# Kernel optimization log

Hardware: AMD Instinct MI355X
Metric: run time of the kernel (lower is better)

The kernel has to match this reference:

```python
import jax, jax.numpy as jnp
import numpy as np

B, T, D, H = 8, 4096, 512, 512


def setup_inputs() -> dict:
    key = jax.random.key(0)
    k1, k2, k3, k4, k5, k6 = jax.random.split(key, 6)
    lim = 1.0 / np.sqrt(D)
    return {
        "x": jax.random.normal(k1, (B, T, D), dtype=jnp.float32),
        "h_0": jax.random.normal(k2, (B, 1, H), dtype=jnp.float32),
        "W_z": jax.random.uniform(k3, (H, D), jnp.float32, -lim, lim),
        "b_z": jax.random.uniform(k4, (H,), jnp.float32, -lim, lim),
        "W_h": jax.random.uniform(k5, (H, D), jnp.float32, -lim, lim),
        "b_h": jax.random.uniform(k6, (H,), jnp.float32, -lim, lim),
    }


def reference(x, h_0, W_z, b_z, W_h, b_h):
    # z_t = sigmoid(W_z x_t), h~_t = tanh(W_h x_t)
    z = jax.nn.sigmoid(jnp.einsum('btd,hd->bth', x, W_z) + b_z)  # (B,T,H)
    h_tilde = jnp.tanh(jnp.einsum('btd,hd->bth', x, W_h) + b_h)  # (B,T,H)
    a = 1.0 - z            # multiplicative coeffs
    b = z * h_tilde        # additive terms (b[:,0] handled as h0 carry)

    # linear recurrence h_t = a_t * h_{t-1} + b_t, h_0 given
    def scan_fn(h_prev, ab):
        a_t, b_t = ab
        h_t = a_t * h_prev + b_t
        return h_t, h_t

    a_t = jnp.swapaxes(a, 0, 1)  # (T,B,H)
    b_t = jnp.swapaxes(b, 0, 1)  # (T,B,H)
    _, hs = jax.lax.scan(scan_fn, h_0[:, 0, :], (a_t, b_t))
    return jnp.swapaxes(hs, 0, 1)  # (B,T,H)
```

## Files before the change

### kernel.cpp

```cpp
#include <hip/hip_runtime.h>

constexpr int Bn = 8, Tn = 4096, Dn = 512, Hn = 512;
constexpr int Mn = Bn * Tn;
constexpr int NKT = Dn / 32;
constexpr int CH = 64, NC = Tn / CH;

typedef __attribute__((ext_vector_type(8))) short s8v;
typedef __attribute__((ext_vector_type(4))) float f4v;
typedef __attribute__((ext_vector_type(8))) _Float16 h8v;
typedef unsigned short ushort_t;

typedef __attribute__((address_space(1))) const void gv_t;
typedef __attribute__((address_space(3))) void lv_t;

__device__ __forceinline__ short f2bf(float f) {
  unsigned u = __float_as_uint(f);
  u = (u + 0x7fffu + ((u >> 16) & 1u)) >> 16;
  return (short)u;
}

__global__ __launch_bounds__(256) void convert_all(
    const float* __restrict__ X, const float* __restrict__ Wz,
    const float* __restrict__ Wh, ushort_t* __restrict__ Xb,
    ushort_t* __restrict__ Wzb, ushort_t* __restrict__ Whb) {
  int bx = blockIdx.x, tid = threadIdx.x;
  const float* src;
  ushort_t* dst;
  int lb;
  if (bx < 4096)      { src = X;  dst = Xb;  lb = bx; }
  else if (bx < 4160) { src = Wz; dst = Wzb; lb = bx - 4096; }
  else                { src = Wh; dst = Whb; lb = bx - 4160; }
  const float* tsrc = src + ((size_t)(lb >> 4) * 128) * Dn + (lb & 15) * 32;
#pragma unroll
  for (int p = 0; p < 2; p++) {
    int idx = tid + p * 256;
    int r = idx >> 2, k8 = idx & 3;
    const float4* sv = reinterpret_cast<const float4*>(tsrc + (size_t)r * Dn + k8 * 8);
    float4 f0 = sv[0], f1 = sv[1];
    s8v v;
    v[0] = f2bf(f0.x); v[1] = f2bf(f0.y); v[2] = f2bf(f0.z); v[3] = f2bf(f0.w);
    v[4] = f2bf(f1.x); v[5] = f2bf(f1.y); v[6] = f2bf(f1.z); v[7] = f2bf(f1.w);
    int c = (r >> 4) * 64 + k8 * 16 + (r & 15);
    *reinterpret_cast<s8v*>(&dst[((size_t)lb * 512 + c) * 8]) = v;
  }
}

__global__ __launch_bounds__(512, 2) void gemm_act(
    const ushort_t* __restrict__ Xb, const ushort_t* __restrict__ Wzb,
    const ushort_t* __restrict__ Whb,
    const float* __restrict__ bzp, const float* __restrict__ bhp,
    h8v* __restrict__ cab, float* __restrict__ cA, float* __restrict__ cB) {
  __shared__ __align__(16) ushort_t lds[2 * 32768];

  int tid = threadIdx.x, lane = tid & 63, wid = tid >> 6;
  int wr = wid >> 1, wc = wid & 1;

  int o = blockIdx.x;
  int wg = (o & 7) * 64 + (o >> 3);
  int bm = wg & 127;
  int bhb = wg >> 7;

  f4v accz[4][4], acch[4][4];
#pragma unroll
  for (int i = 0; i < 4; i++)
#pragma unroll
    for (int j = 0; j < 4; j++) {
      accz[i][j] = (f4v){0.f, 0.f, 0.f, 0.f};
      acch[i][j] = (f4v){0.f, 0.f, 0.f, 0.f};
    }

  auto stage = [&](int buf, int ks) {
    ushort_t* l = lds + buf * 32768;
#pragma unroll
    for (int q = 0; q < 4; q++) {
      const ushort_t* src = Xb + ((size_t)(bm * 2 + (q >> 1)) * 16 + (2 * ks + (q & 1))) * 4096 + tid * 8;
      __builtin_amdgcn_global_load_lds((gv_t*)src, (lv_t*)(l + q * 4096 + tid * 8), 16, 0, 0);
    }
#pragma unroll
    for (int q = 0; q < 2; q++) {
      const ushort_t* sz = Wzb + ((size_t)bhb * 16 + 2 * ks + q) * 4096 + tid * 8;
      __builtin_amdgcn_global_load_lds((gv_t*)sz, (lv_t*)(l + 16384 + q * 4096 + tid * 8), 16, 0, 0);
      const ushort_t* sh = Whb + ((size_t)bhb * 16 + 2 * ks + q) * 4096 + tid * 8;
      __builtin_amdgcn_global_load_lds((gv_t*)sh, (lv_t*)(l + 24576 + q * 4096 + tid * 8), 16, 0, 0);
    }
  };

  stage(0, 0);
  for (int ks = 0; ks < 8; ks++) {
    int cur = ks & 1;
    if (ks < 7) {
      stage(cur ^ 1, ks + 1);
      asm volatile("s_waitcnt vmcnt(8)" ::: "memory");
    } else {
      asm volatile("s_waitcnt vmcnt(0)" ::: "memory");
    }
    __builtin_amdgcn_sched_barrier(0);
    __builtin_amdgcn_s_barrier();
    __builtin_amdgcn_sched_barrier(0);

    const ushort_t* l = lds + cur * 32768;
#pragma unroll
    for (int kk = 0; kk < 2; kk++) {
      s8v af[4], bzf[4], bhf[4];
#pragma unroll
      for (int i = 0; i < 4; i++) {
        int g = wr * 4 + i;
        af[i] = *reinterpret_cast<const s8v*>(&l[(g >> 3) * 8192 + kk * 4096 + (g & 7) * 512 + lane * 8]);
      }
#pragma unroll
      for (int j = 0; j < 4; j++) {
        int gj = wc * 4 + j;
        bzf[j] = *reinterpret_cast<const s8v*>(&l[16384 + kk * 4096 + gj * 512 + lane * 8]);
        bhf[j] = *reinterpret_cast<const s8v*>(&l[24576 + kk * 4096 + gj * 512 + lane * 8]);
      }
      __builtin_amdgcn_s_setprio(1);
#pragma unroll
      for (int i = 0; i < 4; i++)
#pragma unroll
        for (int j = 0; j < 4; j++) {
          accz[i][j] = __builtin_amdgcn_mfma_f32_16x16x32_bf16(af[i], bzf[j], accz[i][j], 0, 0, 0);
          acch[i][j] = __builtin_amdgcn_mfma_f32_16x16x32_bf16(af[i], bhf[j], acch[i][j], 0, 0, 0);
        }
      __builtin_amdgcn_s_setprio(0);
    }
    __builtin_amdgcn_sched_barrier(0);
    __builtin_amdgcn_s_barrier();
  }

  int R = bm * 4 + wr, Cc = bhb * 2 + wc;
  size_t base = (size_t)(R * 8 + Cc) * 1024;
  float bzv[4], bhv[4];
#pragma unroll
  for (int j = 0; j < 4; j++) {
    int h = bhb * 128 + wc * 64 + j * 16 + (lane & 15);
    bzv[j] = bzp[h];
    bhv[j] = bhp[h];
  }
  float QA[4][4], QB[4][4];
#pragma unroll
  for (int i = 0; i < 4; i++)
#pragma unroll
    for (int j = 0; j < 4; j++) {
      h8v g;
      float Pa = 1.f, Pb = 0.f;
#pragma unroll
      for (int q = 0; q < 4; q++) {
        float z = 1.f / (1.f + __expf(-(accz[i][j][q] + bzv[j])));
        float e = __expf(2.f * (acch[i][j][q] + bhv[j]));
        float th = 1.f - 2.f / (e + 1.f);
        g[q] = (_Float16)(1.f - z);
        g[4 + q] = (_Float16)(z * th);
        float a = (float)g[q], b = (float)g[4 + q];
        Pa = a * Pa;
        Pb = a * Pb + b;
      }
      cab[base + (size_t)((i * 4 + j) * 64 + lane)] = g;
      QA[i][j] = Pa;
      QB[i][j] = Pb;
    }

#pragma unroll
  for (int j = 0; j < 4; j++) {
    float A = 1.f, Bv = 0.f;
#pragma unroll
    for (int i = 0; i < 4; i++) {
      float a = QA[i][j], b = QB[i][j];
      float ap = __shfl_xor(a, 16), bp = __shfl_xor(b, 16);
      bool hi = (lane & 16) != 0;
      float af_ = hi ? ap : a, bf_ = hi ? bp : b;
      float as_ = hi ? a : ap, bs_ = hi ? b : bp;
      a = as_ * af_; b = as_ * bf_ + bs_;
      ap = __shfl_xor(a, 32); bp = __shfl_xor(b, 32);
      bool hi2 = (lane & 32) != 0;
      af_ = hi2 ? ap : a; bf_ = hi2 ? bp : b;
      as_ = hi2 ? a : ap; bs_ = hi2 ? b : bp;
      a = as_ * af_; b = as_ * bf_ + bs_;
      Bv = a * Bv + b;
      A = a * A;
    }
    if (lane < 16) {
      int h = bhb * 128 + wc * 64 + j * 16 + lane;
      cA[(size_t)R * Hn + h] = A;
      cB[(size_t)R * Hn + h] = Bv;
    }
  }
}

__global__ __launch_bounds__(256) void scan_heads(
    const float* __restrict__ cA, const float* __restrict__ cB,
    const float* __restrict__ h0p, float* __restrict__ hst) {
  int gid = blockIdx.x * 256 + threadIdx.x;
  int b = gid >> 9, h = gid & 511;
  float hr = h0p[(size_t)b * Hn + h];
#pragma unroll 8
  for (int c = 0; c < NC; c++) {
    size_t o = (size_t)(b * NC + c) * Hn + h;
    hst[o] = hr;
    hr = fmaf(cA[o], hr, cB[o]);
  }
}

__global__ __launch_bounds__(256) void scan_apply(
    const h8v* __restrict__ cab, const float* __restrict__ hst,
    float* __restrict__ out) {
  int h = blockIdx.y * 256 + threadIdx.x;
  int R = blockIdx.x;
  int hl = h & 63, Cc = h >> 6;
  size_t base = (size_t)(R * 8 + Cc) * 1024 + (size_t)(hl >> 4) * 64 + (hl & 15);
  float hr = hst[(size_t)R * Hn + h];
  size_t ob = (size_t)R * 64 * Hn + h;
#pragma unroll
  for (int i = 0; i < 4; i++)
#pragma unroll
    for (int p = 0; p < 4; p++) {
      h8v g = cab[base + i * 256 + p * 16];
#pragma unroll
      for (int q = 0; q < 4; q++) {
        hr = fmaf((float)g[q], hr, (float)g[4 + q]);
        out[ob + (size_t)(i * 16 + p * 4 + q) * Hn] = hr;
      }
    }
}

extern "C" void kernel_launch(void* const* d_in, const int* in_sizes, int n_in,
                              void* d_out, int out_size, void* d_ws, size_t ws_size,
                              hipStream_t stream) {
  const float* X   = (const float*)d_in[0];
  const float* h0p = (const float*)d_in[1];
  const float* Wz  = (const float*)d_in[2];
  const float* bz  = (const float*)d_in[3];
  const float* Wh  = (const float*)d_in[4];
  const float* bh  = (const float*)d_in[5];
  float* out = (float*)d_out;

  char* ws = (char*)d_ws;
  ushort_t* Xb  = (ushort_t*)ws;
  ushort_t* Wzb = Xb + (size_t)Mn * Dn;
  ushort_t* Whb = Wzb + (size_t)Hn * Dn;
  h8v* cab      = (h8v*)(Whb + (size_t)Hn * Dn);
  float* cA     = (float*)(cab + (size_t)Mn * Hn / 4);
  float* cB     = cA + (size_t)Bn * NC * Hn;
  float* hst    = cB + (size_t)Bn * NC * Hn;

  convert_all<<<dim3(4224), 256, 0, stream>>>(X, Wz, Wh, Xb, Wzb, Whb);

  gemm_act<<<dim3(512), 512, 0, stream>>>(Xb, Wzb, Whb, bz, bh, cab, cA, cB);

  scan_heads<<<dim3(Bn * Hn / 256), 256, 0, stream>>>(cA, cB, h0p, hst);
  scan_apply<<<dim3(Mn / 64, Hn / 256), 256, 0, stream>>>(cab, hst, out);
}
```

Measured before the change: 102.0 us.

## Fuse fp32-to-bf16 conversion of X into GEMM staging via registers

The separate conversion pass over X is removed. The GEMM now loads fp32 X rows into registers, converts them with packed bf16 conversion instructions and writes them into LDS in the MFMA layout. Only the weights are still pre-converted. The block-to-tile mapping also changes so that the four H-blocks sharing an X tile run close together, which should improve L2 reuse. This drops a full write and read of the bf16 copy of X, at the cost of more registers, more global read traffic in fp32, and conversion work inside the GEMM main loop.

After: 108.0 us. 1.06x slower.

```diff
diff --git a/kernel.cpp b/kernel.cpp
--- a/kernel.cpp
+++ b/kernel.cpp
@@ -2,7 +2,6 @@
 
 constexpr int Bn = 8, Tn = 4096, Dn = 512, Hn = 512;
 constexpr int Mn = Bn * Tn;
-constexpr int NKT = Dn / 32;
 constexpr int CH = 64, NC = Tn / CH;
 
 typedef __attribute__((ext_vector_type(8))) short s8v;
@@ -19,17 +18,15 @@
   return (short)u;
 }
 
-__global__ __launch_bounds__(256) void convert_all(
-    const float* __restrict__ X, const float* __restrict__ Wz,
-    const float* __restrict__ Wh, ushort_t* __restrict__ Xb,
+__global__ __launch_bounds__(256) void convert_w(
+    const float* __restrict__ Wz, const float* __restrict__ Wh,
     ushort_t* __restrict__ Wzb, ushort_t* __restrict__ Whb) {
   int bx = blockIdx.x, tid = threadIdx.x;
   const float* src;
   ushort_t* dst;
   int lb;
-  if (bx < 4096)      { src = X;  dst = Xb;  lb = bx; }
-  else if (bx < 4160) { src = Wz; dst = Wzb; lb = bx - 4096; }
-  else                { src = Wh; dst = Whb; lb = bx - 4160; }
+  if (bx < 64) { src = Wz; dst = Wzb; lb = bx; }
+  else         { src = Wh; dst = Whb; lb = bx - 64; }
   const float* tsrc = src + ((size_t)(lb >> 4) * 128) * Dn + (lb & 15) * 32;
 #pragma unroll
   for (int p = 0; p < 2; p++) {
@@ -46,7 +43,7 @@
 }
 
 __global__ __launch_bounds__(512, 2) void gemm_act(
-    const ushort_t* __restrict__ Xb, const ushort_t* __restrict__ Wzb,
+    const float* __restrict__ X, const ushort_t* __restrict__ Wzb,
     const ushort_t* __restrict__ Whb,
     const float* __restrict__ bzp, const float* __restrict__ bhp,
     h8v* __restrict__ cab, float* __restrict__ cA, float* __restrict__ cB) {
@@ -56,9 +53,9 @@
   int wr = wid >> 1, wc = wid & 1;
 
   int o = blockIdx.x;
-  int wg = (o & 7) * 64 + (o >> 3);
-  int bm = wg & 127;
-  int bhb = wg >> 7;
+  int x = o & 7, k = o >> 3;
+  int bm = x * 16 + (k >> 2);
+  int bhb = k & 3;
 
   f4v accz[4][4], acch[4][4];
 #pragma unroll
@@ -69,13 +66,16 @@
       acch[i][j] = (f4v){0.f, 0.f, 0.f, 0.f};
     }
 
-  auto stage = [&](int buf, int ks) {
-    ushort_t* l = lds + buf * 32768;
-#pragma unroll
-    for (int q = 0; q < 4; q++) {
-      const ushort_t* src = Xb + ((size_t)(bm * 2 + (q >> 1)) * 16 + (2 * ks + (q & 1))) * 4096 + tid * 8;
-      __builtin_amdgcn_global_load_lds((gv_t*)src, (lv_t*)(l + q * 4096 + tid * 8), 16, 0, 0);
-    }
+  int r = tid >> 1, kh = tid & 1;
+
+  float4 xr[8];
+  auto issueX = [&](int ks) {
+    const float4* s = reinterpret_cast<const float4*>(
+        X + (size_t)(bm * 256 + r) * Dn + ks * 64 + kh * 32);
+#pragma unroll
+    for (int j = 0; j < 8; j++) xr[j] = s[j];
+  };
+  auto issueW = [&](ushort_t* l, int ks) {
 #pragma unroll
     for (int q = 0; q < 2; q++) {
       const ushort_t* sz = Wzb + ((size_t)bhb * 16 + 2 * ks + q) * 4096 + tid * 8;
@@ -84,34 +84,53 @@
       __builtin_amdgcn_global_load_lds((gv_t*)sh, (lv_t*)(l + 24576 + q * 4096 + tid * 8), 16, 0, 0);
     }
   };
-
-  stage(0, 0);
+  auto cvtWrite = [&](ushort_t* l) {
+    const float* f = reinterpret_cast<const float*>(xr);
+    unsigned d[16];
+#pragma unroll
+    for (int n = 0; n < 16; n++) {
+      unsigned dw;
+      asm volatile("v_cvt_pk_bf16_f32 %0, %1, %2" : "=v"(dw) : "v"(f[2 * n]), "v"(f[2 * n + 1]));
+      d[n] = dw;
+    }
+    int cb = (r >> 7) * 1024 + kh * 512 + ((r >> 4) & 7) * 64 + (r & 15);
+#pragma unroll
+    for (int q = 0; q < 4; q++) {
+      uint4 w = {d[4 * q], d[4 * q + 1], d[4 * q + 2], d[4 * q + 3]};
+      *reinterpret_cast<uint4*>(&l[(size_t)(cb + q * 16) * 8]) = w;
+    }
+  };
+
+  issueX(0);
+  issueW(lds, 0);
+  asm volatile("s_waitcnt vmcnt(4)" ::: "memory");
+  cvtWrite(lds);
+  asm volatile("s_waitcnt vmcnt(0) lgkmcnt(0)" ::: "memory");
+  __builtin_amdgcn_sched_barrier(0);
+  __builtin_amdgcn_s_barrier();
+
   for (int ks = 0; ks < 8; ks++) {
-    int cur = ks & 1;
+    ushort_t* lc = lds + (ks & 1) * 32768;
+    ushort_t* ln = lds + ((ks & 1) ^ 1) * 32768;
     if (ks < 7) {
-      stage(cur ^ 1, ks + 1);
-      asm volatile("s_waitcnt vmcnt(8)" ::: "memory");
-    } else {
-      asm volatile("s_waitcnt vmcnt(0)" ::: "memory");
+      issueX(ks + 1);
+      issueW(ln, ks + 1);
     }
     __builtin_amdgcn_sched_barrier(0);
-    __builtin_amdgcn_s_barrier();
-    __builtin_amdgcn_sched_barrier(0);
-
-    const ushort_t* l = lds + cur * 32768;
+
 #pragma unroll
     for (int kk = 0; kk < 2; kk++) {
       s8v af[4], bzf[4], bhf[4];
 #pragma unroll
       for (int i = 0; i < 4; i++) {
         int g = wr * 4 + i;
-        af[i] = *reinterpret_cast<const s8v*>(&l[(g >> 3) * 8192 + kk * 4096 + (g & 7) * 512 + lane * 8]);
+        af[i] = *reinterpret_cast<const s8v*>(&lc[(g >> 3) * 8192 + kk * 4096 + (g & 7) * 512 + lane * 8]);
       }
 #pragma unroll
       for (int j = 0; j < 4; j++) {
         int gj = wc * 4 + j;
-        bzf[j] = *reinterpret_cast<const s8v*>(&l[16384 + kk * 4096 + gj * 512 + lane * 8]);
-        bhf[j] = *reinterpret_cast<const s8v*>(&l[24576 + kk * 4096 + gj * 512 + lane * 8]);
+        bzf[j] = *reinterpret_cast<const s8v*>(&lc[16384 + kk * 4096 + gj * 512 + lane * 8]);
+        bhf[j] = *reinterpret_cast<const s8v*>(&lc[24576 + kk * 4096 + gj * 512 + lane * 8]);
       }
       __builtin_amdgcn_s_setprio(1);
 #pragma unroll
@@ -123,6 +142,13 @@
         }
       __builtin_amdgcn_s_setprio(0);
     }
+
+    if (ks < 7) {
+      asm volatile("s_waitcnt vmcnt(4)" ::: "memory");
+      cvtWrite(ln);
+      asm volatile("s_waitcnt vmcnt(0)" ::: "memory");
+    }
+    asm volatile("s_waitcnt lgkmcnt(0)" ::: "memory");
     __builtin_amdgcn_sched_barrier(0);
     __builtin_amdgcn_s_barrier();
   }
@@ -234,17 +260,16 @@
   float* out = (float*)d_out;
 
   char* ws = (char*)d_ws;
-  ushort_t* Xb  = (ushort_t*)ws;
-  ushort_t* Wzb = Xb + (size_t)Mn * Dn;
+  ushort_t* Wzb = (ushort_t*)ws;
   ushort_t* Whb = Wzb + (size_t)Hn * Dn;
   h8v* cab      = (h8v*)(Whb + (size_t)Hn * Dn);
   float* cA     = (float*)(cab + (size_t)Mn * Hn / 4);
   float* cB     = cA + (size_t)Bn * NC * Hn;
   float* hst    = cB + (size_t)Bn * NC * Hn;
 
-  convert_all<<<dim3(4224), 256, 0, stream>>>(X, Wz, Wh, Xb, Wzb, Whb);
-
-  gemm_act<<<dim3(512), 512, 0, stream>>>(Xb, Wzb, Whb, bz, bh, cab, cA, cB);
+  convert_w<<<dim3(128), 256, 0, stream>>>(Wz, Wh, Wzb, Whb);
+
+  gemm_act<<<dim3(512), 512, 0, stream>>>(X, Wzb, Whb, bz, bh, cab, cA, cB);
 
   scan_heads<<<dim3(Bn * Hn / 256), 256, 0, stream>>>(cA, cB, h0p, hst);
   scan_apply<<<dim3(Mn / 64, Hn / 256), 256, 0, stream>>>(cab, hst, out);
```

## Keep 64-column weight slice resident in LDS and stream X fragments from global

Applied to the files above, without the earlier changes.

The GEMM kernel now loads a block's full Wz/Wh slice for 64 hidden columns (all K) into LDS once, then each wave reads its own A fragments directly from global memory with register double-buffering. This removes the per-K-step barriers and the LDS staging of X. The tile shape changes from 128 columns by 4 row tiles to 64 columns by 8 row tiles per block. The cost is redundant global reads of X across the 8 column blocks and exposed global latency in the MFMA loop. The conversion kernel is also split into separate X and weight launches.

After: 95.66 us. 6.2% less time.

```diff
diff --git a/kernel.cpp b/kernel.cpp
--- a/kernel.cpp
+++ b/kernel.cpp
@@ -2,7 +2,6 @@
 
 constexpr int Bn = 8, Tn = 4096, Dn = 512, Hn = 512;
 constexpr int Mn = Bn * Tn;
-constexpr int NKT = Dn / 32;
 constexpr int CH = 64, NC = Tn / CH;
 
 typedef __attribute__((ext_vector_type(8))) short s8v;
@@ -19,17 +18,33 @@
   return (short)u;
 }
 
-__global__ __launch_bounds__(256) void convert_all(
-    const float* __restrict__ X, const float* __restrict__ Wz,
-    const float* __restrict__ Wh, ushort_t* __restrict__ Xb,
+__global__ __launch_bounds__(256) void convert_x(
+    const float* __restrict__ X, ushort_t* __restrict__ Xb) {
+  int lb = blockIdx.x, tid = threadIdx.x;
+  const float* tsrc = X + ((size_t)(lb >> 4) * 128) * Dn + (lb & 15) * 32;
+#pragma unroll
+  for (int p = 0; p < 2; p++) {
+    int idx = tid + p * 256;
+    int r = idx >> 2, k8 = idx & 3;
+    const float4* sv = reinterpret_cast<const float4*>(tsrc + (size_t)r * Dn + k8 * 8);
+    float4 f0 = sv[0], f1 = sv[1];
+    s8v v;
+    v[0] = f2bf(f0.x); v[1] = f2bf(f0.y); v[2] = f2bf(f0.z); v[3] = f2bf(f0.w);
+    v[4] = f2bf(f1.x); v[5] = f2bf(f1.y); v[6] = f2bf(f1.z); v[7] = f2bf(f1.w);
+    int c = (r >> 4) * 64 + k8 * 16 + (r & 15);
+    *reinterpret_cast<s8v*>(&Xb[((size_t)lb * 512 + c) * 8]) = v;
+  }
+}
+
+__global__ __launch_bounds__(256) void convert_w(
+    const float* __restrict__ Wz, const float* __restrict__ Wh,
     ushort_t* __restrict__ Wzb, ushort_t* __restrict__ Whb) {
   int bx = blockIdx.x, tid = threadIdx.x;
   const float* src;
   ushort_t* dst;
   int lb;
-  if (bx < 4096)      { src = X;  dst = Xb;  lb = bx; }
-  else if (bx < 4160) { src = Wz; dst = Wzb; lb = bx - 4096; }
-  else                { src = Wh; dst = Whb; lb = bx - 4160; }
+  if (bx < 64) { src = Wz; dst = Wzb; lb = bx; }
+  else         { src = Wh; dst = Whb; lb = bx - 64; }
   const float* tsrc = src + ((size_t)(lb >> 4) * 128) * Dn + (lb & 15) * 32;
 #pragma unroll
   for (int p = 0; p < 2; p++) {
@@ -50,15 +65,23 @@
     const ushort_t* __restrict__ Whb,
     const float* __restrict__ bzp, const float* __restrict__ bhp,
     h8v* __restrict__ cab, float* __restrict__ cA, float* __restrict__ cB) {
-  __shared__ __align__(16) ushort_t lds[2 * 32768];
+  __shared__ __align__(16) ushort_t lds[32 * 2048];
 
   int tid = threadIdx.x, lane = tid & 63, wid = tid >> 6;
-  int wr = wid >> 1, wc = wid & 1;
 
   int o = blockIdx.x;
-  int wg = (o & 7) * 64 + (o >> 3);
-  int bm = wg & 127;
-  int bhb = wg >> 7;
+  int loc = o >> 3;
+  int mt = (o & 7) * 8 + (loc >> 3);
+  int p = loc & 7;
+
+#pragma unroll
+  for (int q = 0; q < 16; q++) {
+    int r = q * 2 + (wid >> 2);
+    int kt = r & 15;
+    const ushort_t* wsrc = (r >= 16 ? Whb : Wzb);
+    const ushort_t* s = wsrc + ((size_t)((p >> 1) * 16 + kt)) * 4096 + (p & 1) * 2048 + (tid & 255) * 8;
+    __builtin_amdgcn_global_load_lds((gv_t*)s, (lv_t*)(lds + r * 2048 + (tid & 255) * 8), 16, 0, 0);
+  }
 
   f4v accz[4][4], acch[4][4];
 #pragma unroll
@@ -69,70 +92,61 @@
       acch[i][j] = (f4v){0.f, 0.f, 0.f, 0.f};
     }
 
-  auto stage = [&](int buf, int ks) {
-    ushort_t* l = lds + buf * 32768;
-#pragma unroll
-    for (int q = 0; q < 4; q++) {
-      const ushort_t* src = Xb + ((size_t)(bm * 2 + (q >> 1)) * 16 + (2 * ks + (q & 1))) * 4096 + tid * 8;
-      __builtin_amdgcn_global_load_lds((gv_t*)src, (lv_t*)(l + q * 4096 + tid * 8), 16, 0, 0);
-    }
-#pragma unroll
-    for (int q = 0; q < 2; q++) {
-      const ushort_t* sz = Wzb + ((size_t)bhb * 16 + 2 * ks + q) * 4096 + tid * 8;
-      __builtin_amdgcn_global_load_lds((gv_t*)sz, (lv_t*)(l + 16384 + q * 4096 + tid * 8), 16, 0, 0);
-      const ushort_t* sh = Whb + ((size_t)bhb * 16 + 2 * ks + q) * 4096 + tid * 8;
-      __builtin_amdgcn_global_load_lds((gv_t*)sh, (lv_t*)(l + 24576 + q * 4096 + tid * 8), 16, 0, 0);
+  int rw = mt * 8 + wid;
+  int rt = rw >> 1, half = rw & 1;
+  const ushort_t* xb = Xb + (size_t)rt * 16 * 4096;
+
+  __syncthreads();
+
+  auto ldW = [&](int kt, s8v* bzf, s8v* bhf) {
+#pragma unroll
+    for (int j = 0; j < 4; j++) {
+      bzf[j] = *reinterpret_cast<const s8v*>(lds + (size_t)kt * 2048 + (j * 64 + lane) * 8);
+      bhf[j] = *reinterpret_cast<const s8v*>(lds + (size_t)(16 + kt) * 2048 + (j * 64 + lane) * 8);
     }
   };
-
-  stage(0, 0);
-  for (int ks = 0; ks < 8; ks++) {
-    int cur = ks & 1;
-    if (ks < 7) {
-      stage(cur ^ 1, ks + 1);
-      asm volatile("s_waitcnt vmcnt(8)" ::: "memory");
-    } else {
-      asm volatile("s_waitcnt vmcnt(0)" ::: "memory");
-    }
-    __builtin_amdgcn_sched_barrier(0);
-    __builtin_amdgcn_s_barrier();
-    __builtin_amdgcn_sched_barrier(0);
-
-    const ushort_t* l = lds + cur * 32768;
-#pragma unroll
-    for (int kk = 0; kk < 2; kk++) {
-      s8v af[4], bzf[4], bhf[4];
-#pragma unroll
-      for (int i = 0; i < 4; i++) {
-        int g = wr * 4 + i;
-        af[i] = *reinterpret_cast<const s8v*>(&l[(g >> 3) * 8192 + kk * 4096 + (g & 7) * 512 + lane * 8]);
+  auto mfmaStep = [&](s8v* af, s8v* bzf, s8v* bhf) {
+    __builtin_amdgcn_s_setprio(1);
+#pragma unroll
+    for (int i = 0; i < 4; i++)
+#pragma unroll
+      for (int j = 0; j < 4; j++) {
+        accz[i][j] = __builtin_amdgcn_mfma_f32_16x16x32_bf16(af[i], bzf[j], accz[i][j], 0, 0, 0);
+        acch[i][j] = __builtin_amdgcn_mfma_f32_16x16x32_bf16(af[i], bhf[j], acch[i][j], 0, 0, 0);
       }
-#pragma unroll
-      for (int j = 0; j < 4; j++) {
-        int gj = wc * 4 + j;
-        bzf[j] = *reinterpret_cast<const s8v*>(&l[16384 + kk * 4096 + gj * 512 + lane * 8]);
-        bhf[j] = *reinterpret_cast<const s8v*>(&l[24576 + kk * 4096 + gj * 512 + lane * 8]);
-      }
-      __builtin_amdgcn_s_setprio(1);
+    __builtin_amdgcn_s_setprio(0);
+  };
+
+  s8v afA[4], afB[4];
+#pragma unroll
+  for (int i = 0; i < 4; i++)
+    afA[i] = *reinterpret_cast<const s8v*>(xb + ((half * 4 + i) * 64 + lane) * 8);
+
+#pragma unroll
+  for (int kp = 0; kp < 8; kp++) {
+    int k0 = 2 * kp;
+#pragma unroll
+    for (int i = 0; i < 4; i++)
+      afB[i] = *reinterpret_cast<const s8v*>(xb + (size_t)(k0 + 1) * 4096 + ((half * 4 + i) * 64 + lane) * 8);
+    s8v bz0[4], bh0[4];
+    ldW(k0, bz0, bh0);
+    mfmaStep(afA, bz0, bh0);
+    if (k0 + 2 < 16) {
 #pragma unroll
       for (int i = 0; i < 4; i++)
-#pragma unroll
-        for (int j = 0; j < 4; j++) {
-          accz[i][j] = __builtin_amdgcn_mfma_f32_16x16x32_bf16(af[i], bzf[j], accz[i][j], 0, 0, 0);
-          acch[i][j] = __builtin_amdgcn_mfma_f32_16x16x32_bf16(af[i], bhf[j], acch[i][j], 0, 0, 0);
-        }
-      __builtin_amdgcn_s_setprio(0);
-    }
-    __builtin_amdgcn_sched_barrier(0);
-    __builtin_amdgcn_s_barrier();
-  }
-
-  int R = bm * 4 + wr, Cc = bhb * 2 + wc;
+        afA[i] = *reinterpret_cast<const s8v*>(xb + (size_t)(k0 + 2) * 4096 + ((half * 4 + i) * 64 + lane) * 8);
+    }
+    s8v bz1[4], bh1[4];
+    ldW(k0 + 1, bz1, bh1);
+    mfmaStep(afB, bz1, bh1);
+  }
+
+  int R = rw, Cc = p;
   size_t base = (size_t)(R * 8 + Cc) * 1024;
   float bzv[4], bhv[4];
 #pragma unroll
   for (int j = 0; j < 4; j++) {
-    int h = bhb * 128 + wc * 64 + j * 16 + (lane & 15);
+    int h = p * 64 + j * 16 + (lane & 15);
     bzv[j] = bzp[h];
     bhv[j] = bhp[h];
   }
@@ -179,7 +193,7 @@
       A = a * A;
     }
     if (lane < 16) {
-      int h = bhb * 128 + wc * 64 + j * 16 + lane;
+      int h = p * 64 + j * 16 + lane;
       cA[(size_t)R * Hn + h] = A;
       cB[(size_t)R * Hn + h] = Bv;
     }
@@ -242,7 +256,8 @@
   float* cB     = cA + (size_t)Bn * NC * Hn;
   float* hst    = cB + (size_t)Bn * NC * Hn;
 
-  convert_all<<<dim3(4224), 256, 0, stream>>>(X, Wz, Wh, Xb, Wzb, Whb);
+  convert_x<<<dim3(4096), 256, 0, stream>>>(X, Xb);
+  convert_w<<<dim3(128), 256, 0, stream>>>(Wz, Wh, Wzb, Whb);
 
   gemm_act<<<dim3(512), 512, 0, stream>>>(Xb, Wzb, Whb, bz, bh, cab, cA, cB);
 
```
